# Kernel tuning notes

Hardware: AMD Instinct MI355X
Metric: run time of the kernel (lower is better)

Reference implementation:

```python
import jax, jax.numpy as jnp
import numpy as np

N, Z_DIM = 131072, 64
K_CODES = 2048
QUANT_TEMP = 0.0  # default T when 'quant_temp' not passed


def setup_inputs() -> dict:
    key = jax.random.key(0)
    k1, k2 = jax.random.split(key)
    z = jax.random.normal(k1, (N, Z_DIM), dtype=jnp.float32)
    e = jax.random.normal(k2, (K_CODES, Z_DIM), dtype=jnp.float32)
    return {"z": z, "e": e}


def reference(z, e):
    # torch.cdist -> euclidean distance matrix [N, K]; argmin over squared
    # distance gives identical indices (sqrt is monotone), so skip the sqrt.
    # ||z - e||^2 = ||z||^2 - 2 z.e^T + ||e||^2
    z_sq = jnp.sum(z * z, axis=1, keepdims=True)          # [N, 1]
    e_sq = jnp.sum(e * e, axis=1)                          # [K]
    d2 = z_sq - 2.0 * (z @ e.T) + e_sq[None, :]            # [N, K]
    min_indices = jnp.argmin(d2, axis=1)                   # [N] int
    z_q = e[min_indices]                                   # gather [N, Z]
    commit_loss = jnp.mean((z - z_q) ** 2)                 # F.mse_loss
    # straight-through: z + (1 - T) * stop_grad(z_q - z), T = 0
    z_out = z + (1.0 - QUANT_TEMP) * jax.lax.stop_gradient(z_q - z)
    return z_out, min_indices, commit_loss
```

## Files before the change

### kernel.cpp

```cpp
#include <hip/hip_runtime.h>


#define N_ROWS 131072
#define ZD 64
#define KCODES 2048
#define RF 4
#define EPS_S 0.02f
#define FLAG_CAP 65536
#define RFIX 4

using f16x8   = __attribute__((ext_vector_type(8))) _Float16;
using floatx4 = __attribute__((ext_vector_type(4))) float;


__global__ void prep_kernel(const float* __restrict__ e, float* __restrict__ ws) {
    int t = threadIdx.x, lane = t & 63, w = t >> 6;
    if (blockIdx.x == 0 && t == 0) { ws[0] = 0.0f; ((unsigned int*)ws)[1] = 0u; }
    int c = blockIdx.x * 4 + w;
    float* esn = ws + 1024;
    double* esq64 = (double*)((char*)ws + 16384);
    unsigned short* et = (unsigned short*)((char*)ws + 32768);
    float* eT = (float*)((char*)ws + 557056);

    float x = e[(size_t)c * ZD + lane];
    union { _Float16 h; unsigned short u; } cv;
    cv.h = (_Float16)x;
    int base = ((c >> 4) << 10) + ((lane >> 3) << 7) + ((c & 15) << 3) + (lane & 7);
    et[base] = cv.u;
    eT[lane * KCODES + c] = x;
    double s = (double)x * (double)x;
    for (int off = 1; off < 64; off <<= 1) s += __shfl_xor(s, off, 64);
    if (lane == 0) { esq64[c] = s; esn[c] = (float)(-0.5 * s); }
}

#define COMPUTE(H0, H1, EN, FCOL) do {                                       \
    floatx4 _ai = {EN, EN, EN, EN};                                          \
    _Pragma("unroll")                                                        \
    for (int _rf = 0; _rf < RF; _rf++) {                                     \
        floatx4 acc;                                                         \
        acc = __builtin_amdgcn_mfma_f32_16x16x32_f16(Fh[_rf][0], H0, _ai, 0, 0, 0); \
        acc = __builtin_amdgcn_mfma_f32_16x16x32_f16(Fh[_rf][1], H1, acc, 0, 0, 0); \
        _Pragma("unroll")                                                    \
        for (int _r = 0; _r < 4; _r++) {                                     \
            float _s  = acc[_r];                                             \
            bool  _gt = _s > mval[_rf][_r];                                  \
            mv2[_rf][_r]  = __builtin_amdgcn_fmed3f(_s, mval[_rf][_r], mv2[_rf][_r]); \
            midx[_rf][_r] = _gt ? (FCOL) : midx[_rf][_r];                    \
            mval[_rf][_r] = fmaxf(_s, mval[_rf][_r]);                        \
        }                                                                    \
    }                                                                        \
} while (0)

#define STAGEP(BUF, P) do {                                                  \
    const char* _src = etiles + ((size_t)((P) & 63) << 12)                   \
                       + ((size_t)threadIdx.x << 4);                         \
    __builtin_amdgcn_global_load_lds(                                        \
        (const __attribute__((address_space(1))) unsigned int*)_src,         \
        (__attribute__((address_space(3))) unsigned int*)&tilebuf[BUF][w << 10], \
        16, 0, 0);                                                           \
} while (0)

#define ITER2(BUF, P) do {                                                   \
    STAGEP((BUF) ^ 1, (P) + 1);                                              \
    float _en0 = esn_sm[(P) * 32 + lrow];                                    \
    float _en1 = esn_sm[(P) * 32 + 16 + lrow];                               \
    f16x8 h0, h1;                                                            \
    h0 = *(const f16x8*)(const void*)(tilebuf[BUF] + (lane << 4));           \
    h1 = *(const f16x8*)(const void*)(tilebuf[BUF] + 1024 + (lane << 4));    \
    COMPUTE(h0, h1, _en0, fcol);                                             \
    fcol += 16.0f;                                                           \
    h0 = *(const f16x8*)(const void*)(tilebuf[BUF] + 2048 + (lane << 4));    \
    h1 = *(const f16x8*)(const void*)(tilebuf[BUF] + 3072 + (lane << 4));    \
    COMPUTE(h0, h1, _en1, fcol);                                             \
    fcol += 16.0f;                                                           \
    __syncthreads();                                                         \
} while (0)

__global__ __launch_bounds__(256, 2) void vq_mfma(
        const float* __restrict__ z, const float* __restrict__ e,
        float* __restrict__ ws, float* __restrict__ out) {
    const char* etiles = (const char*)ws + 32768;
    unsigned int* cntp  = (unsigned int*)ws + 1;
    unsigned int* flags = (unsigned int*)((char*)ws + 294912);

    __shared__ __attribute__((aligned(16))) char tilebuf[2][4096];
    __shared__ __attribute__((aligned(16))) float esn_sm[KCODES];

    int lane = threadIdx.x & 63;
    int w    = threadIdx.x >> 6;
    int wid  = blockIdx.x * 4 + w;
    int row0 = wid * (RF * 16);
    int lrow = lane & 15;
    int lq   = lane >> 4;

    f16x8 Fh[RF][2];
#pragma unroll
    for (int rf = 0; rf < RF; rf++)
#pragma unroll
        for (int kc = 0; kc < 2; kc++) {
            const float* zp = z + (size_t)(row0 + rf * 16 + lrow) * ZD + kc * 32 + lq * 8;
            float xv[8];
            *(float4*)(void*)&xv[0] = *(const float4*)(const void*)zp;
            *(float4*)(void*)&xv[4] = *(const float4*)(const void*)(zp + 4);
            f16x8 h;
#pragma unroll
            for (int j = 0; j < 8; j++) h[j] = (_Float16)xv[j];
            Fh[rf][kc] = h;
            asm volatile("" : "+v"(Fh[rf][kc]));
        }

    {
        const char* esrc = (const char*)ws + 4096 + ((size_t)threadIdx.x << 4);
        __builtin_amdgcn_global_load_lds(
            (const __attribute__((address_space(1))) unsigned int*)esrc,
            (__attribute__((address_space(3))) unsigned int*)((char*)esn_sm + (w << 10)),
            16, 0, 0);
        __builtin_amdgcn_global_load_lds(
            (const __attribute__((address_space(1))) unsigned int*)(esrc + 4096),
            (__attribute__((address_space(3))) unsigned int*)((char*)esn_sm + 4096 + (w << 10)),
            16, 0, 0);
    }
    STAGEP(0, 0);

    floatx4 mval[RF], mv2[RF], midx[RF];
#pragma unroll
    for (int rf = 0; rf < RF; rf++)
#pragma unroll
        for (int r = 0; r < 4; r++) {
            mval[rf][r] = -3.0e38f; mv2[rf][r] = -3.0e38f; midx[rf][r] = 0.0f;
        }

    float fcol = (float)lrow;
    __syncthreads();

    for (int p = 0; p < 64; p += 2) {
        ITER2(0, p);
        ITER2(1, p + 1);
    }

    float lacc = 0.0f;
#pragma unroll
    for (int rf = 0; rf < RF; rf++)
#pragma unroll
        for (int r = 0; r < 4; r++) {
            float v = mval[rf][r], v2 = mv2[rf][r], fi = midx[rf][r];
            for (int off = 1; off < 16; off <<= 1) {
                float ov  = __shfl_xor(v,  off, 64);
                float ofi = __shfl_xor(fi, off, 64);
                float ov2 = __shfl_xor(v2, off, 64);
                bool take = (ov > v) || ((ov == v) && (ofi < fi));
                float loser = take ? v : ov;
                v2 = fmaxf(fmaxf(v2, ov2), loser);
                v  = take ? ov  : v;
                fi = take ? ofi : fi;
            }
            int row = row0 + rf * 16 + lq * 4 + r;
            int idx = (int)fi;
            float4 ev = ((const float4*)(const void*)(e + (size_t)idx * ZD))[lrow];
            float4 zv = ((const float4*)(const void*)(z + (size_t)row * ZD))[lrow];
            ((float4*)(void*)(out + (size_t)row * ZD))[lrow] = ev;
            float dx = ev.x - zv.x, dy = ev.y - zv.y;
            float dz = ev.z - zv.z, dw = ev.w - zv.w;
            lacc = fmaf(dx, dx, lacc); lacc = fmaf(dy, dy, lacc);
            lacc = fmaf(dz, dz, lacc); lacc = fmaf(dw, dw, lacc);
            if (lrow == 0) {
                out[(size_t)N_ROWS * ZD + row] = fi;
                if (v - v2 < EPS_S) {
                    unsigned int i = atomicAdd(cntp, 1u);
                    if (i < FLAG_CAP) flags[i] = (unsigned int)row;
                }
            }
        }

    for (int off = 1; off < 64; off <<= 1) lacc += __shfl_xor(lacc, off, 64);
    __shared__ float sm[4];
    if (lane == 0) sm[w] = lacc;
    __syncthreads();
    if (threadIdx.x == 0) atomicAdd(ws, sm[0] + sm[1] + sm[2] + sm[3]);
}

__global__ __launch_bounds__(256) void vq_fixup(
        const float* __restrict__ z, const float* __restrict__ e,
        float* __restrict__ ws, float* __restrict__ out) {
    const double* esq64 = (const double*)((const char*)ws + 16384);
    const float* eT = (const float*)((const char*)ws + 557056);
    const unsigned int* flags = (const unsigned int*)((const char*)ws + 294912);
    unsigned int cnt = ((const unsigned int*)ws)[1];
    bool allrows = cnt > FLAG_CAP;
    unsigned int n = allrows ? N_ROWS : cnt;

    if (blockIdx.x == 0 && threadIdx.x == 0)
        out[(size_t)N_ROWS * ZD + N_ROWS] = ws[0] * (1.0f / 8388608.0f);
    if (n == 0) return;

    __shared__ float zrow[RFIX][ZD];
    __shared__ int rows_sm[RFIX];
    __shared__ double sd[4][RFIX]; __shared__ int si[4][RFIX];
    __shared__ int sbest[RFIX];
    int t = threadIdx.x, lane = t & 63, w = t >> 6;

    unsigned int ngroups = (n + RFIX - 1) / RFIX;
    for (unsigned int g = blockIdx.x; g < ngroups; g += gridDim.x) {
        __syncthreads();
        if (t < RFIX) {
            unsigned int u = g * RFIX + (unsigned int)t;
            if (u >= n) u = n - 1;
            rows_sm[t] = allrows ? (int)u : (int)flags[u];
        }
        __syncthreads();
        zrow[t >> 6][t & 63] = z[(size_t)rows_sm[t >> 6] * ZD + (t & 63)];
        __syncthreads();

        double dacc[8][RFIX];
#pragma unroll
        for (int j = 0; j < 8; j++)
#pragma unroll
            for (int r = 0; r < RFIX; r++) dacc[j][r] = 0.0;

        for (int k = 0; k < ZD; k++) {
            const float* ek = eT + k * KCODES + t;
            float e8[8];
#pragma unroll
            for (int j = 0; j < 8; j++) e8[j] = ek[256 * j];
#pragma unroll
            for (int r = 0; r < RFIX; r++) {
                double zk = (double)zrow[r][k];
#pragma unroll
                for (int j = 0; j < 8; j++)
                    dacc[j][r] = fma(zk, (double)e8[j], dacc[j][r]);
            }
        }

#pragma unroll
        for (int r = 0; r < RFIX; r++) {
            double dmin = 1.0e300; int imin = 0;
#pragma unroll
            for (int j = 0; j < 8; j++) {
                int c = t + 256 * j;
                double d = fma(-2.0, dacc[j][r], esq64[c]);
                if (d < dmin) { dmin = d; imin = c; }
            }
            for (int off = 1; off < 64; off <<= 1) {
                double od = __shfl_xor(dmin, off, 64);
                int    oi = __shfl_xor(imin, off, 64);
                if (od < dmin || (od == dmin && oi < imin)) { dmin = od; imin = oi; }
            }
            if (lane == 0) { sd[w][r] = dmin; si[w][r] = imin; }
        }
        __syncthreads();
        if (t < RFIX) {
            double bd = sd[0][t]; int bi = si[0][t];
            for (int q = 1; q < 4; q++)
                if (sd[q][t] < bd || (sd[q][t] == bd && si[q][t] < bi)) {
                    bd = sd[q][t]; bi = si[q][t];
                }
            sbest[t] = bi;
        }
        __syncthreads();
        if (t < 16 * RFIX) {
            int r = t >> 4, pos = t & 15;
            unsigned int u = g * RFIX + (unsigned int)r;
            if (u < n) {
                int row = rows_sm[r]; int bi = sbest[r];
                ((float4*)(void*)(out + (size_t)row * ZD))[pos] =
                    ((const float4*)(const void*)(e + (size_t)bi * ZD))[pos];
                if (pos == 0) out[(size_t)N_ROWS * ZD + row] = (float)bi;
            }
        }
    }
}

extern "C" void kernel_launch(void* const* d_in, const int* in_sizes, int n_in,
                              void* d_out, int out_size, void* d_ws, size_t ws_size,
                              hipStream_t stream) {
    const float* z = (const float*)d_in[0];
    const float* e = (const float*)d_in[1];
    float* out = (float*)d_out;
    float* ws  = (float*)d_ws;

    prep_kernel<<<dim3(512), dim3(256), 0, stream>>>(e, ws);
    vq_mfma<<<dim3(512), dim3(256), 0, stream>>>(z, e, ws, out);
    vq_fixup<<<dim3(1024), dim3(256), 0, stream>>>(z, e, ws, out);
}
```

Measured before the change: 182.8 us.

## Deepen codebook tile pipeline to four LDS buffers with prefetch distance two

The main VQ kernel moves from a double-buffered LDS tile ring with a full __syncthreads after each tile to a four-slot ring that prefetches two tiles ahead. It waits with an explicit s_waitcnt vmcnt(2) plus s_barrier, which keeps more global-to-LDS loads in flight and lets the wait for the current tile overlap with later loads. The fix-up kernel also processes 8 rows per group instead of 4, so each transposed-codebook load is reused across more rows. The cost is extra LDS per block (which may affect occupancy), more double accumulators in the fix-up kernel, and reliance on hand-written vmcnt counting being correct.

```diff
diff --git a/kernel.cpp b/kernel.cpp
--- a/kernel.cpp
+++ b/kernel.cpp
@@ -7,7 +7,7 @@
 #define RF 4
 #define EPS_S 0.02f
 #define FLAG_CAP 65536
-#define RFIX 4
+#define RFIX 8
 
 using f16x8   = __attribute__((ext_vector_type(8))) _Float16;
 using floatx4 = __attribute__((ext_vector_type(4))) float;
@@ -60,20 +60,22 @@
         16, 0, 0);                                                           \
 } while (0)
 
-#define ITER2(BUF, P) do {                                                   \
-    STAGEP((BUF) ^ 1, (P) + 1);                                              \
-    float _en0 = esn_sm[(P) * 32 + lrow];                                    \
-    float _en1 = esn_sm[(P) * 32 + 16 + lrow];                               \
+#define ITER_R(CT) do {                                                      \
+    STAGEP(((CT) + 2) & 3, (CT) + 2);                                        \
+    asm volatile("s_waitcnt vmcnt(2)" ::: "memory");                         \
+    __builtin_amdgcn_s_barrier();                                            \
+    float _en0 = esn_sm[(CT) * 32 + lrow];                                   \
+    float _en1 = esn_sm[(CT) * 32 + 16 + lrow];                              \
+    const char* _tb = tilebuf[(CT) & 3];                                     \
     f16x8 h0, h1;                                                            \
-    h0 = *(const f16x8*)(const void*)(tilebuf[BUF] + (lane << 4));           \
-    h1 = *(const f16x8*)(const void*)(tilebuf[BUF] + 1024 + (lane << 4));    \
+    h0 = *(const f16x8*)(const void*)(_tb + (lane << 4));                    \
+    h1 = *(const f16x8*)(const void*)(_tb + 1024 + (lane << 4));             \
     COMPUTE(h0, h1, _en0, fcol);                                             \
     fcol += 16.0f;                                                           \
-    h0 = *(const f16x8*)(const void*)(tilebuf[BUF] + 2048 + (lane << 4));    \
-    h1 = *(const f16x8*)(const void*)(tilebuf[BUF] + 3072 + (lane << 4));    \
+    h0 = *(const f16x8*)(const void*)(_tb + 2048 + (lane << 4));             \
+    h1 = *(const f16x8*)(const void*)(_tb + 3072 + (lane << 4));             \
     COMPUTE(h0, h1, _en1, fcol);                                             \
     fcol += 16.0f;                                                           \
-    __syncthreads();                                                         \
 } while (0)
 
 __global__ __launch_bounds__(256, 2) void vq_mfma(
@@ -83,7 +85,7 @@
     unsigned int* cntp  = (unsigned int*)ws + 1;
     unsigned int* flags = (unsigned int*)((char*)ws + 294912);
 
-    __shared__ __attribute__((aligned(16))) char tilebuf[2][4096];
+    __shared__ __attribute__((aligned(16))) char tilebuf[4][4096];
     __shared__ __attribute__((aligned(16))) float esn_sm[KCODES];
 
     int lane = threadIdx.x & 63;
@@ -108,6 +110,7 @@
             Fh[rf][kc] = h;
             asm volatile("" : "+v"(Fh[rf][kc]));
         }
+    asm volatile("s_waitcnt vmcnt(0)" ::: "memory");
 
     {
         const char* esrc = (const char*)ws + 4096 + ((size_t)threadIdx.x << 4);
@@ -121,6 +124,7 @@
             16, 0, 0);
     }
     STAGEP(0, 0);
+    STAGEP(1, 1);
 
     floatx4 mval[RF], mv2[RF], midx[RF];
 #pragma unroll
@@ -131,11 +135,12 @@
         }
 
     float fcol = (float)lrow;
-    __syncthreads();
-
-    for (int p = 0; p < 64; p += 2) {
-        ITER2(0, p);
-        ITER2(1, p + 1);
+
+    for (int ct = 0; ct < 64; ct += 4) {
+        ITER_R(ct);
+        ITER_R(ct + 1);
+        ITER_R(ct + 2);
+        ITER_R(ct + 3);
     }
 
     float lacc = 0.0f;
@@ -208,7 +213,8 @@
             rows_sm[t] = allrows ? (int)u : (int)flags[u];
         }
         __syncthreads();
-        zrow[t >> 6][t & 63] = z[(size_t)rows_sm[t >> 6] * ZD + (t & 63)];
+        zrow[t >> 6][t & 63]       = z[(size_t)rows_sm[t >> 6] * ZD + (t & 63)];
+        zrow[4 + (t >> 6)][t & 63] = z[(size_t)rows_sm[4 + (t >> 6)] * ZD + (t & 63)];
         __syncthreads();
 
         double dacc[8][RFIX];
```

Result: slower. 192.0 us (+5.0%).
